# Performance work log

Measured on AMD Instinct MI355X. Metric: run time of the kernel, lower is better.

The kernel has to match this reference:

```python
import jax, jax.numpy as jnp
import numpy as np

N = 100000   # nodes per type
D = 128      # embedding_dim
H = 4        # attn_heads
C = D // H   # out_channels
E = 400000   # edges per relation
NEG_SLOPE = 0.01  # F.leaky_relu default


def setup_inputs() -> dict:
    key = jax.random.key(0)
    ks = jax.random.split(key, 24)
    inp = {
        "featA": jax.random.normal(ks[0], (N, D), jnp.float32),
        "featB": jax.random.normal(ks[1], (N, D), jnp.float32),
        "src_aa": jax.random.randint(ks[2], (E,), 0, N, jnp.int32),
        "dst_aa": jax.random.randint(ks[3], (E,), 0, N, jnp.int32),
        "src_ab": jax.random.randint(ks[4], (E,), 0, N, jnp.int32),
        "dst_ab": jax.random.randint(ks[5], (E,), 0, N, jnp.int32),
        "src_ba": jax.random.randint(ks[6], (E,), 0, N, jnp.int32),
        "dst_ba": jax.random.randint(ks[7], (E,), 0, N, jnp.int32),
    }
    # per-layer params: W stacked over node types [A=0, B=1]; attn over metapaths [aa=0, ab=1, ba=2]
    i = 8
    for t in range(2):
        inp[f"Wl{t}"] = jax.random.normal(ks[i + 0], (2, D, D), jnp.float32) * 0.05
        inp[f"bl{t}"] = jnp.zeros((2, D), jnp.float32)
        inp[f"Wr{t}"] = jax.random.normal(ks[i + 1], (2, D, D), jnp.float32) * 0.05
        inp[f"br{t}"] = jnp.zeros((2, D), jnp.float32)
        inp[f"al{t}"] = jax.random.normal(ks[i + 2], (3, H, C), jnp.float32) * 0.1
        inp[f"ar{t}"] = jax.random.normal(ks[i + 3], (3, H, C), jnp.float32) * 0.1
        i += 4
    return inp


def _segment_softmax(att, dst, n):
    # att: [E, H]; softmax over incoming edges per destination node, per head
    m = jax.ops.segment_max(att, dst, num_segments=n)
    e = jnp.exp(att - m[dst])
    s = jax.ops.segment_sum(e, dst, num_segments=n)
    return e / s[dst]


def _relation(k_src, v_dst, src, dst, a_l, a_r, n_dst):
    # per-edge attention: leaky_relu((k_src*attn_l).sum + (v_dst*attn_r).sum)
    att = jax.nn.leaky_relu((k_src[src] * a_l).sum(-1) + (v_dst[dst] * a_r).sum(-1), NEG_SLOPE)  # [E,H]
    alpha = _segment_softmax(att, dst, n_dst)                                                    # [E,H]
    # message h = v of the DESTINATION node (as in edge_attention), weighted-summed per dst
    h = jax.ops.segment_sum(alpha[..., None] * v_dst[dst], dst, num_segments=n_dst)              # [Nd,H,C]
    return h.reshape(n_dst, -1)


def _layer(hA, hB, Wl, bl, Wr, br, al, ar, edges):
    src_aa, dst_aa, src_ab, dst_ab, src_ba, dst_ba = edges
    kA = (hA @ Wl[0] + bl[0]).reshape(N, H, C)
    kB = (hB @ Wl[1] + bl[1]).reshape(N, H, C)
    vA = (hA @ Wr[0] + br[0]).reshape(N, H, C)
    vB = (hB @ Wr[1] + br[1]).reshape(N, H, C)
    h_aa = _relation(kA, vA, src_aa, dst_aa, al[0], ar[0], N)  # A -> A
    h_ab = _relation(kA, vB, src_ab, dst_ab, al[1], ar[1], N)  # A -> B
    h_ba = _relation(kB, vA, src_ba, dst_ba, al[2], ar[2], N)  # B -> A
    # mean over stacked relation outputs + the node's own v, then relu
    outA = jax.nn.relu((h_aa + h_ba + vA.reshape(N, D)) / 3.0)
    outB = jax.nn.relu((h_ab + vB.reshape(N, D)) / 2.0)
    return outA, outB


def reference(featA, featB, src_aa, dst_aa, src_ab, dst_ab, src_ba, dst_ba,
              Wl0, bl0, Wr0, br0, al0, ar0, Wl1, bl1, Wr1, br1, al1, ar1):
    edges = (src_aa, dst_aa, src_ab, dst_ab, src_ba, dst_ba)
    hA, hB = _layer(featA, featB, Wl0, bl0, Wr0, br0, al0, ar0, edges)
    hA, hB = _layer(hA, hB, Wl1, bl1, Wr1, br1, al1, ar1, edges)
    return jnp.stack([hA, hB])  # [2, N, D]
```

## Files before the change

kernel.cpp:

```cpp
#include <hip/hip_runtime.h>
#include <hip/hip_bf16.h>

#define NN 100000
#define DD 128
#define EE 400000

typedef unsigned short u16;
typedef __attribute__((ext_vector_type(4))) float floatx4;
typedef __attribute__((ext_vector_type(8))) short shortx8;

__device__ __forceinline__ u16 f2bf(float f) {
    unsigned u = __float_as_uint(f);
    u += 0x7FFFu + ((u >> 16) & 1u);
    return (u16)(u >> 16);
}

__global__ void mark_deg(const int* __restrict__ daa, const int* __restrict__ dab,
                         const int* __restrict__ dba,
                         unsigned char* __restrict__ maa, unsigned char* __restrict__ mab,
                         unsigned char* __restrict__ mba) {
    int e = blockIdx.x * 256 + threadIdx.x;
    if (e < EE) {
        maa[daa[e]] = 1;
        mab[dab[e]] = 1;
        mba[dba[e]] = 1;
    }
}

__global__ void make_scales(const unsigned char* __restrict__ maa,
                            const unsigned char* __restrict__ mab,
                            const unsigned char* __restrict__ mba,
                            float* __restrict__ sA, float* __restrict__ sB) {
    int n = blockIdx.x * 256 + threadIdx.x;
    if (n < NN) {
        sA[n] = (1.0f + (float)maa[n] + (float)mba[n]) * (1.0f / 3.0f);
        sB[n] = (1.0f + (float)mab[n]) * 0.5f;
    }
}

__global__ void conv_wt(const float* __restrict__ Wr0, const float* __restrict__ Wr1,
                        u16* __restrict__ Wt) {
    int idx = blockIdx.x * 256 + threadIdx.x;
    int mat = idx >> 14;
    int n = (idx >> 7) & 127;
    int k = idx & 127;
    const float* W = (mat < 2) ? (Wr0 + mat * 16384) : (Wr1 + (mat - 2) * 16384);
    Wt[idx] = f2bf(W[k * 128 + n]);
}

template <bool IN_BF16, bool OUT_BF16>
__global__ __launch_bounds__(256) void gemm_rowscale(
    const void* __restrict__ Ain, const u16* __restrict__ Wt,
    const float* __restrict__ bias, const float* __restrict__ scale,
    void* __restrict__ out) {
    __shared__ u16 Wlds[128 * 136];
    const int t = threadIdx.x;
#pragma unroll
    for (int i = 0; i < 8; ++i) {
        int idx = i * 256 + t;
        int n = idx >> 4, c8 = idx & 15;
        shortx8 v = ((const shortx8*)Wt)[idx];
        *(shortx8*)&Wlds[n * 136 + c8 * 8] = v;
    }
    __syncthreads();

    const int wave = t >> 6;
    const int lane = t & 63;
    const int quad = lane >> 4;
    const int mrow = lane & 15;
    const int m0 = blockIdx.x * 64 + wave * 16;
    const int m = m0 + mrow;
    const int msafe = (m < NN) ? m : (NN - 1);

    shortx8 afrag[4];
    if constexpr (IN_BF16) {
        const u16* arow = (const u16*)Ain + (size_t)msafe * 128;
#pragma unroll
        for (int ks = 0; ks < 4; ++ks)
            afrag[ks] = *(const shortx8*)(arow + ks * 32 + quad * 8);
    } else {
        const float* arow = (const float*)Ain + (size_t)msafe * 128;
#pragma unroll
        for (int ks = 0; ks < 4; ++ks) {
            floatx4 f0 = *(const floatx4*)(arow + ks * 32 + quad * 8);
            floatx4 f1 = *(const floatx4*)(arow + ks * 32 + quad * 8 + 4);
            union { shortx8 v; u16 u[8]; } uu;
            uu.u[0] = f2bf(f0[0]); uu.u[1] = f2bf(f0[1]);
            uu.u[2] = f2bf(f0[2]); uu.u[3] = f2bf(f0[3]);
            uu.u[4] = f2bf(f1[0]); uu.u[5] = f2bf(f1[1]);
            uu.u[6] = f2bf(f1[2]); uu.u[7] = f2bf(f1[3]);
            afrag[ks] = uu.v;
        }
    }

    floatx4 acc[8];
#pragma unroll
    for (int nt = 0; nt < 8; ++nt) acc[nt] = (floatx4){0.f, 0.f, 0.f, 0.f};

#pragma unroll
    for (int ks = 0; ks < 4; ++ks) {
#pragma unroll
        for (int nt = 0; nt < 8; ++nt) {
            shortx8 b = *(const shortx8*)&Wlds[(nt * 16 + mrow) * 136 + ks * 32 + quad * 8];
            acc[nt] = __builtin_amdgcn_mfma_f32_16x16x32_bf16(afrag[ks], b, acc[nt], 0, 0, 0);
        }
    }

    float scl[4];
    int orow[4];
#pragma unroll
    for (int r = 0; r < 4; ++r) {
        orow[r] = m0 + quad * 4 + r;
        scl[r] = scale[(orow[r] < NN) ? orow[r] : (NN - 1)];
    }
#pragma unroll
    for (int nt = 0; nt < 8; ++nt) {
        int col = nt * 16 + mrow;
        float bv = bias[col];
#pragma unroll
        for (int r = 0; r < 4; ++r) {
            if (orow[r] < NN) {
                float v = (acc[nt][r] + bv) * scl[r];
                v = fmaxf(v, 0.0f);
                if constexpr (OUT_BF16)
                    ((u16*)out)[(size_t)orow[r] * 128 + col] = f2bf(v);
                else
                    ((float*)out)[(size_t)orow[r] * 128 + col] = v;
            }
        }
    }
}

extern "C" void kernel_launch(void* const* d_in, const int* in_sizes, int n_in,
                              void* d_out, int out_size, void* d_ws, size_t ws_size,
                              hipStream_t stream) {
    (void)in_sizes; (void)n_in; (void)out_size;
    const float* featA = (const float*)d_in[0];
    const float* featB = (const float*)d_in[1];
    const int* dst_aa = (const int*)d_in[3];
    const int* dst_ab = (const int*)d_in[5];
    const int* dst_ba = (const int*)d_in[7];
    const float* Wr0 = (const float*)d_in[10];
    const float* br0 = (const float*)d_in[11];
    const float* Wr1 = (const float*)d_in[16];
    const float* br1 = (const float*)d_in[17];

    char* ws = (char*)d_ws;
    size_t o = 0;
    u16* Wt = (u16*)(ws + o);           o += (size_t)4 * 16384 * 2;
    float* sA = (float*)(ws + o);       o += (size_t)NN * 4;
    float* sB = (float*)(ws + o);       o += (size_t)NN * 4;
    unsigned char* masks = (unsigned char*)(ws + o); o += (size_t)3 * NN;
    o = (o + 255) & ~(size_t)255;
    u16* hA1 = (u16*)(ws + o);
    u16* hB1 = hA1 + (size_t)NN * 128;
    const bool big = ws_size >= o + (size_t)2 * NN * 128 * 2;

    float* outA = (float*)d_out;
    float* outB = outA + (size_t)NN * 128;

    hipMemsetAsync(masks, 0, (size_t)3 * NN, stream);
    mark_deg<<<(EE + 255) / 256, 256, 0, stream>>>(dst_aa, dst_ab, dst_ba,
                                                   masks, masks + NN, masks + 2 * NN);
    make_scales<<<(NN + 255) / 256, 256, 0, stream>>>(masks, masks + NN, masks + 2 * NN, sA, sB);
    conv_wt<<<256, 256, 0, stream>>>(Wr0, Wr1, Wt);

    const int gb = (NN + 63) / 64;
    if (big) {
        gemm_rowscale<false, true><<<gb, 256, 0, stream>>>(featA, Wt, br0, sA, hA1);
        gemm_rowscale<false, true><<<gb, 256, 0, stream>>>(featB, Wt + 16384, br0 + 128, sB, hB1);
        gemm_rowscale<true, false><<<gb, 256, 0, stream>>>(hA1, Wt + 2 * 16384, br1, sA, outA);
        gemm_rowscale<true, false><<<gb, 256, 0, stream>>>(hB1, Wt + 3 * 16384, br1 + 128, sB, outB);
    } else {
        gemm_rowscale<false, false><<<gb, 256, 0, stream>>>(featA, Wt, br0, sA, outA);
        gemm_rowscale<false, false><<<gb, 256, 0, stream>>>(featB, Wt + 16384, br0 + 128, sB, outB);
        gemm_rowscale<false, false><<<gb, 256, 0, stream>>>(outA, Wt + 2 * 16384, br1, sA, outA);
        gemm_rowscale<false, false><<<gb, 256, 0, stream>>>(outB, Wt + 3 * 16384, br1 + 128, sB, outB);
    }
}
```

Baseline: 289.9 us.

## Fuse both layer GEMMs per node type with LDS-resident intermediate and merged prep

Replaces the four per-layer GEMM launches with one kernel that computes layer 1, stages the bf16 activations in LDS, and immediately runs layer 2, removing the global round-trip of the intermediate. The mask marking, scale computation and weight conversion are merged into a single prep kernel, and scales are derived on the fly from the masks. This cuts launches and memory traffic, at the cost of larger LDS use per block and extra block-level synchronisation.

```diff
diff --git a/kernel.cpp b/kernel.cpp
--- a/kernel.cpp
+++ b/kernel.cpp
@@ -2,8 +2,8 @@
 #include <hip/hip_bf16.h>
 
 #define NN 100000
-#define DD 128
 #define EE 400000
+#define NPAD 136
 
 typedef unsigned short u16;
 typedef __attribute__((ext_vector_type(4))) float floatx4;
@@ -15,71 +15,69 @@
     return (u16)(u >> 16);
 }
 
-__global__ void mark_deg(const int* __restrict__ daa, const int* __restrict__ dab,
-                         const int* __restrict__ dba,
-                         unsigned char* __restrict__ maa, unsigned char* __restrict__ mab,
-                         unsigned char* __restrict__ mba) {
-    int e = blockIdx.x * 256 + threadIdx.x;
-    if (e < EE) {
-        maa[daa[e]] = 1;
-        mab[dab[e]] = 1;
-        mba[dba[e]] = 1;
+__global__ __launch_bounds__(256) void prep(
+    const int* __restrict__ daa, const int* __restrict__ dab, const int* __restrict__ dba,
+    unsigned char* __restrict__ masks,
+    const float* __restrict__ Wr0, const float* __restrict__ Wr1,
+    u16* __restrict__ Wt) {
+    int b = blockIdx.x;
+    int t = threadIdx.x;
+    if (b < (EE + 255) / 256) {
+        int e = b * 256 + t;
+        if (e < EE) {
+            masks[daa[e]] = 1;
+            masks[NN + dab[e]] = 1;
+            masks[2 * NN + dba[e]] = 1;
+        }
+    } else {
+        int idx = (b - (EE + 255) / 256) * 256 + t;
+        int mat = idx >> 14;
+        int n = (idx >> 7) & 127;
+        int k = idx & 127;
+        const float* W = (mat < 2) ? (Wr0 + mat * 16384) : (Wr1 + (mat - 2) * 16384);
+        Wt[idx] = f2bf(W[k * 128 + n]);
     }
 }
 
-__global__ void make_scales(const unsigned char* __restrict__ maa,
-                            const unsigned char* __restrict__ mab,
-                            const unsigned char* __restrict__ mba,
-                            float* __restrict__ sA, float* __restrict__ sB) {
-    int n = blockIdx.x * 256 + threadIdx.x;
-    if (n < NN) {
-        sA[n] = (1.0f + (float)maa[n] + (float)mba[n]) * (1.0f / 3.0f);
-        sB[n] = (1.0f + (float)mab[n]) * 0.5f;
-    }
-}
+__global__ __launch_bounds__(512, 4) void fused2(
+    const float* __restrict__ featA, const float* __restrict__ featB,
+    const u16* __restrict__ Wt,
+    const float* __restrict__ br0, const float* __restrict__ br1,
+    const unsigned char* __restrict__ masks,
+    float* __restrict__ out) {
+    __shared__ u16 ldsW0[128 * NPAD];
+    __shared__ u16 ldsW1[128 * NPAD];
 
-__global__ void conv_wt(const float* __restrict__ Wr0, const float* __restrict__ Wr1,
-                        u16* __restrict__ Wt) {
-    int idx = blockIdx.x * 256 + threadIdx.x;
-    int mat = idx >> 14;
-    int n = (idx >> 7) & 127;
-    int k = idx & 127;
-    const float* W = (mat < 2) ? (Wr0 + mat * 16384) : (Wr1 + (mat - 2) * 16384);
-    Wt[idx] = f2bf(W[k * 128 + n]);
-}
+    const int blocksPerType = (NN + 127) / 128;
+    const int type = (blockIdx.x >= blocksPerType) ? 1 : 0;
+    const int blk = blockIdx.x - type * blocksPerType;
+    const float* feat = type ? featB : featA;
+    const u16* W0 = Wt + type * 16384;
+    const u16* W1 = Wt + (2 + type) * 16384;
+    const float* b0 = br0 + type * 128;
+    const float* b1 = br1 + type * 128;
+    float* outp = out + (size_t)type * NN * 128;
 
-template <bool IN_BF16, bool OUT_BF16>
-__global__ __launch_bounds__(256) void gemm_rowscale(
-    const void* __restrict__ Ain, const u16* __restrict__ Wt,
-    const float* __restrict__ bias, const float* __restrict__ scale,
-    void* __restrict__ out) {
-    __shared__ u16 Wlds[128 * 136];
     const int t = threadIdx.x;
 #pragma unroll
-    for (int i = 0; i < 8; ++i) {
-        int idx = i * 256 + t;
+    for (int i = 0; i < 4; ++i) {
+        int idx = i * 512 + t;
         int n = idx >> 4, c8 = idx & 15;
-        shortx8 v = ((const shortx8*)Wt)[idx];
-        *(shortx8*)&Wlds[n * 136 + c8 * 8] = v;
+        *(shortx8*)&ldsW0[n * NPAD + c8 * 8] = ((const shortx8*)W0)[idx];
+        *(shortx8*)&ldsW1[n * NPAD + c8 * 8] = ((const shortx8*)W1)[idx];
     }
-    __syncthreads();
 
     const int wave = t >> 6;
     const int lane = t & 63;
     const int quad = lane >> 4;
     const int mrow = lane & 15;
-    const int m0 = blockIdx.x * 64 + wave * 16;
+    const int m0 = blk * 128 + wave * 16;
     const int m = m0 + mrow;
     const int msafe = (m < NN) ? m : (NN - 1);
 
     shortx8 afrag[4];
-    if constexpr (IN_BF16) {
-        const u16* arow = (const u16*)Ain + (size_t)msafe * 128;
-#pragma unroll
-        for (int ks = 0; ks < 4; ++ks)
-            afrag[ks] = *(const shortx8*)(arow + ks * 32 + quad * 8);
-    } else {
-        const float* arow = (const float*)Ain + (size_t)msafe * 128;
+    {
+        const float* arow = feat + (size_t)msafe * 128;
 #pragma unroll
         for (int ks = 0; ks < 4; ++ks) {
             floatx4 f0 = *(const floatx4*)(arow + ks * 32 + quad * 8);
@@ -93,40 +91,67 @@
         }
     }
 
+    float scl[4];
+#pragma unroll
+    for (int r = 0; r < 4; ++r) {
+        int rr = m0 + quad * 4 + r;
+        rr = (rr < NN) ? rr : (NN - 1);
+        scl[r] = type ? (1.0f + (float)masks[NN + rr]) * 0.5f
+                      : (1.0f + (float)masks[rr] + (float)masks[2 * NN + rr]) * (1.0f / 3.0f);
+    }
+
+    __syncthreads();
+
     floatx4 acc[8];
 #pragma unroll
     for (int nt = 0; nt < 8; ++nt) acc[nt] = (floatx4){0.f, 0.f, 0.f, 0.f};
-
 #pragma unroll
-    for (int ks = 0; ks < 4; ++ks) {
+    for (int ks = 0; ks < 4; ++ks)
 #pragma unroll
         for (int nt = 0; nt < 8; ++nt) {
-            shortx8 b = *(const shortx8*)&Wlds[(nt * 16 + mrow) * 136 + ks * 32 + quad * 8];
-            acc[nt] = __builtin_amdgcn_mfma_f32_16x16x32_bf16(afrag[ks], b, acc[nt], 0, 0, 0);
+            shortx8 bfr = *(const shortx8*)&ldsW0[(nt * 16 + mrow) * NPAD + ks * 32 + quad * 8];
+            acc[nt] = __builtin_amdgcn_mfma_f32_16x16x32_bf16(afrag[ks], bfr, acc[nt], 0, 0, 0);
         }
-    }
 
-    float scl[4];
-    int orow[4];
-#pragma unroll
-    for (int r = 0; r < 4; ++r) {
-        orow[r] = m0 + quad * 4 + r;
-        scl[r] = scale[(orow[r] < NN) ? orow[r] : (NN - 1)];
-    }
+    __syncthreads();
+
 #pragma unroll
     for (int nt = 0; nt < 8; ++nt) {
         int col = nt * 16 + mrow;
-        float bv = bias[col];
+        float bv = b0[col];
 #pragma unroll
         for (int r = 0; r < 4; ++r) {
-            if (orow[r] < NN) {
-                float v = (acc[nt][r] + bv) * scl[r];
-                v = fmaxf(v, 0.0f);
-                if constexpr (OUT_BF16)
-                    ((u16*)out)[(size_t)orow[r] * 128 + col] = f2bf(v);
-                else
-                    ((float*)out)[(size_t)orow[r] * 128 + col] = v;
-            }
+            float v = fmaxf((acc[nt][r] + bv) * scl[r], 0.0f);
+            ldsW0[(wave * 16 + quad * 4 + r) * NPAD + col] = f2bf(v);
+        }
+    }
+    __syncthreads();
+
+    shortx8 a2[4];
+#pragma unroll
+    for (int ks = 0; ks < 4; ++ks)
+        a2[ks] = *(const shortx8*)&ldsW0[(wave * 16 + mrow) * NPAD + ks * 32 + quad * 8];
+
+    floatx4 acc2[8];
+#pragma unroll
+    for (int nt = 0; nt < 8; ++nt) acc2[nt] = (floatx4){0.f, 0.f, 0.f, 0.f};
+#pragma unroll
+    for (int ks = 0; ks < 4; ++ks)
+#pragma unroll
+        for (int nt = 0; nt < 8; ++nt) {
+            shortx8 bfr = *(const shortx8*)&ldsW1[(nt * 16 + mrow) * NPAD + ks * 32 + quad * 8];
+            acc2[nt] = __builtin_amdgcn_mfma_f32_16x16x32_bf16(a2[ks], bfr, acc2[nt], 0, 0, 0);
+        }
+
+#pragma unroll
+    for (int nt = 0; nt < 8; ++nt) {
+        int col = nt * 16 + mrow;
+        float bv = b1[col];
+#pragma unroll
+        for (int r = 0; r < 4; ++r) {
+            int row = m0 + quad * 4 + r;
+            if (row < NN)
+                outp[(size_t)row * 128 + col] = fmaxf((acc2[nt][r] + bv) * scl[r], 0.0f);
         }
     }
 }
@@ -134,7 +159,7 @@
 extern "C" void kernel_launch(void* const* d_in, const int* in_sizes, int n_in,
                               void* d_out, int out_size, void* d_ws, size_t ws_size,
                               hipStream_t stream) {
-    (void)in_sizes; (void)n_in; (void)out_size;
+    (void)in_sizes; (void)n_in; (void)out_size; (void)ws_size;
     const float* featA = (const float*)d_in[0];
     const float* featB = (const float*)d_in[1];
     const int* dst_aa = (const int*)d_in[3];
@@ -146,35 +171,14 @@
     const float* br1 = (const float*)d_in[17];
 
     char* ws = (char*)d_ws;
-    size_t o = 0;
-    u16* Wt = (u16*)(ws + o);           o += (size_t)4 * 16384 * 2;
-    float* sA = (float*)(ws + o);       o += (size_t)NN * 4;
-    float* sB = (float*)(ws + o);       o += (size_t)NN * 4;
-    unsigned char* masks = (unsigned char*)(ws + o); o += (size_t)3 * NN;
-    o = (o + 255) & ~(size_t)255;
-    u16* hA1 = (u16*)(ws + o);
-    u16* hB1 = hA1 + (size_t)NN * 128;
-    const bool big = ws_size >= o + (size_t)2 * NN * 128 * 2;
-
-    float* outA = (float*)d_out;
-    float* outB = outA + (size_t)NN * 128;
+    u16* Wt = (u16*)ws;
+    unsigned char* masks = (unsigned char*)(ws + 4 * 16384 * 2);
 
     hipMemsetAsync(masks, 0, (size_t)3 * NN, stream);
-    mark_deg<<<(EE + 255) / 256, 256, 0, stream>>>(dst_aa, dst_ab, dst_ba,
-                                                   masks, masks + NN, masks + 2 * NN);
-    make_scales<<<(NN + 255) / 256, 256, 0, stream>>>(masks, masks + NN, masks + 2 * NN, sA, sB);
-    conv_wt<<<256, 256, 0, stream>>>(Wr0, Wr1, Wt);
+    const int markBlocks = (EE + 255) / 256;
+    prep<<<markBlocks + 256, 256, 0, stream>>>(dst_aa, dst_ab, dst_ba, masks, Wr0, Wr1, Wt);
 
-    const int gb = (NN + 63) / 64;
-    if (big) {
-        gemm_rowscale<false, true><<<gb, 256, 0, stream>>>(featA, Wt, br0, sA, hA1);
-        gemm_rowscale<false, true><<<gb, 256, 0, stream>>>(featB, Wt + 16384, br0 + 128, sB, hB1);
-        gemm_rowscale<true, false><<<gb, 256, 0, stream>>>(hA1, Wt + 2 * 16384, br1, sA, outA);
-        gemm_rowscale<true, false><<<gb, 256, 0, stream>>>(hB1, Wt + 3 * 16384, br1 + 128, sB, outB);
-    } else {
-        gemm_rowscale<false, false><<<gb, 256, 0, stream>>>(featA, Wt, br0, sA, outA);
-        gemm_rowscale<false, false><<<gb, 256, 0, stream>>>(featB, Wt + 16384, br0 + 128, sB, outB);
-        gemm_rowscale<false, false><<<gb, 256, 0, stream>>>(outA, Wt + 2 * 16384, br1, sA, outA);
-        gemm_rowscale<false, false><<<gb, 256, 0, stream>>>(outB, Wt + 3 * 16384, br1 + 128, sB, outB);
-    }
+    const int blocksPerType = (NN + 127) / 128;
+    fused2<<<2 * blocksPerType, 512, 0, stream>>>(featA, featB, Wt, br0, br1, masks,
+                                                  (float*)d_out);
 }
```

Result: faster. 253.9 us (-12.4%).
